# Optimization experiments

Hardware: AMD Instinct MI355X
Metric: run time of the kernel (lower is better)

Reference implementation:

```python
import jax, jax.numpy as jnp
import numpy as np

N_HEAD = 16
D_HEAD = 64
N_GROUPS = 4
D_EMBED = 1024
ROPE_N = 32
B, T = 2, 2048


def apply_rope(x, cos, sin):
    # x: (..., T, ROPE_N); cos/sin: (T, ROPE_N) broadcast over leading dims
    h = x.shape[-1]
    x1, x2 = x[..., : h // 2], x[..., h // 2 :]
    rotated = jnp.concatenate((-x2, x1), axis=-1)
    return (x * cos + rotated * sin).astype(x.dtype)


def setup_inputs() -> dict:
    key = jax.random.key(0)
    k1, k2, k3, k4, k5 = jax.random.split(key, 5)
    return {
        "x": jax.random.normal(k1, (B, T, D_EMBED), dtype=jnp.float32),
        "cos": jax.random.uniform(k2, (T, ROPE_N), dtype=jnp.float32),
        "sin": jax.random.uniform(k3, (T, ROPE_N), dtype=jnp.float32),
        "mask": jnp.ones((B, T), dtype=bool),  # unused by the original forward (passes None to SDPA)
        "Wqkv": jax.random.normal(k4, (D_EMBED, (N_HEAD + 2 * N_GROUPS) * D_HEAD), dtype=jnp.float32) * 0.02,
        "Wout": jax.random.normal(k5, (N_HEAD * D_HEAD, D_EMBED), dtype=jnp.float32) * 0.02,
    }


def reference(x, cos, sin, mask, Wqkv, Wout):
    Bv, Tv, _ = x.shape
    q_per_kv = N_HEAD // N_GROUPS  # 4
    total_qkv = q_per_kv + 2       # 6

    qkv = jnp.einsum("btc,cf->btf", x, Wqkv)  # (B, T, 1536)
    qkv = qkv.reshape(Bv, Tv, N_GROUPS, total_qkv, D_HEAD)
    qkv = jnp.transpose(qkv, (0, 2, 3, 1, 4))  # (B, G, total_qkv, T, d)

    q = qkv[:, :, :q_per_kv]           # (B, G, q_per_kv, T, d)
    k = qkv[:, :, q_per_kv : q_per_kv + 1]  # (B, G, 1, T, d)
    v = qkv[:, :, q_per_kv + 1 :]           # (B, G, 1, T, d)

    # GQA expand (1 < groups < heads)
    k = jnp.broadcast_to(k, (Bv, N_GROUPS, q_per_kv, Tv, D_HEAD))
    v = jnp.broadcast_to(v, (Bv, N_GROUPS, q_per_kv, Tv, D_HEAD))

    q = q.reshape(Bv, N_HEAD, Tv, D_HEAD)
    k = k.reshape(Bv, N_HEAD, Tv, D_HEAD)
    v = v.reshape(Bv, N_HEAD, Tv, D_HEAD)

    # partial RoPE on the first ROPE_N dims of each head
    q = jnp.concatenate((apply_rope(q[..., :ROPE_N], cos, sin), q[..., ROPE_N:]), axis=-1)
    k = jnp.concatenate((apply_rope(k[..., :ROPE_N], cos, sin), k[..., ROPE_N:]), axis=-1)

    scale = 1.0 / np.sqrt(D_HEAD).astype(np.float32)
    scores = jnp.einsum("bhtd,bhsd->bhts", q, k) * scale
    attn = jax.nn.softmax(scores, axis=-1)
    y = jnp.einsum("bhts,bhsd->bhtd", attn, v)   # (B, H, T, d)
    y = jnp.transpose(y, (0, 2, 1, 3)).reshape(Bv, Tv, N_HEAD * D_HEAD)
    return jnp.einsum("btf,fc->btc", y, Wout)
```

## Files before the change

kernel.cpp:

```cpp
#include <hip/hip_runtime.h>
#include <hip/hip_bf16.h>
#include <math.h>

#define BATCH   2
#define TSEQ    2048
#define DEMBED  1024
#define NHEAD   16
#define DHEAD   64
#define NGROUP  4
#define ROPEN   32
#define FQKV    1536
#define MROWS   (BATCH*TSEQ)

typedef __attribute__((ext_vector_type(8))) short short8;
typedef __attribute__((ext_vector_type(4))) float floatx4;

__device__ __forceinline__ void split_pack8(const float* f, uint4& h4, uint4& l4) {
    uint u[8], lu[8];
    #pragma unroll
    for (int j = 0; j < 8; ++j) {
        u[j] = __float_as_uint(f[j]);
        float lf = f[j] - __uint_as_float(u[j] & 0xffff0000u);
        lu[j] = __float_as_uint(lf);
    }
    h4.x = __builtin_amdgcn_perm(u[1], u[0], 0x07060302u);
    h4.y = __builtin_amdgcn_perm(u[3], u[2], 0x07060302u);
    h4.z = __builtin_amdgcn_perm(u[5], u[4], 0x07060302u);
    h4.w = __builtin_amdgcn_perm(u[7], u[6], 0x07060302u);
    l4.x = __builtin_amdgcn_perm(lu[1], lu[0], 0x07060302u);
    l4.y = __builtin_amdgcn_perm(lu[3], lu[2], 0x07060302u);
    l4.z = __builtin_amdgcn_perm(lu[5], lu[4], 0x07060302u);
    l4.w = __builtin_amdgcn_perm(lu[7], lu[6], 0x07060302u);
}

__device__ __forceinline__ void rtn_pack8(const float* f, uint4& h4) {
    uint t[8];
    #pragma unroll
    for (int j = 0; j < 8; ++j)
        t[j] = __float_as_uint(f[j]) + 0x8000u;
    h4.x = __builtin_amdgcn_perm(t[1], t[0], 0x07060302u);
    h4.y = __builtin_amdgcn_perm(t[3], t[2], 0x07060302u);
    h4.z = __builtin_amdgcn_perm(t[5], t[4], 0x07060302u);
    h4.w = __builtin_amdgcn_perm(t[7], t[6], 0x07060302u);
}

__device__ __forceinline__ uint pk_bf16x2(float f0, float f1) {
    uint u0 = __float_as_uint(f0) + 0x8000u;
    uint u1 = __float_as_uint(f1) + 0x8000u;
    return __builtin_amdgcn_perm(u1, u0, 0x07060302u);
}

__device__ __forceinline__ float fast_exp2(float x) {
    float r;
    asm("v_exp_f32 %0, %1" : "=v"(r) : "v"(x));
    return r;
}

__device__ __forceinline__ void lds_async16(void* lds, const void* gp) {
    __builtin_amdgcn_global_load_lds(
        (const __attribute__((address_space(1))) unsigned int*)gp,
        (__attribute__((address_space(3))) unsigned int*)lds,
        16, 0, 0);
}


__global__ __launch_bounds__(256) void conv_xy(const float* __restrict__ in,
                                               char* __restrict__ img) {
    const int tid = threadIdx.x;
    const int c   = blockIdx.x & 15;
    const int mt  = blockIdx.x >> 4;
    const int r    = tid >> 1;
    const int half = tid & 1;

    const float* src = in + (size_t)(mt*128 + r)*1024 + c*64 + half*32;
    float f[32];
    #pragma unroll
    for (int u = 0; u < 8; ++u)
        *(float4*)(f + 4*u) = *(const float4*)(src + 4*u);

    char* tile = img + ((size_t)(mt*16 + c)) * 32768;
    #pragma unroll
    for (int cc = 0; cc < 4; ++cc) {
        uint4 h4, l4;
        split_pack8(f + cc*8, h4, l4);
        int j    = half*4 + cc;
        int phys = j ^ (r & 7);
        *(uint4*)(tile + r*128 + phys*16)         = h4;
        *(uint4*)(tile + 16384 + r*128 + phys*16) = l4;
    }
}

__global__ __launch_bounds__(256) void conv_w(const float* __restrict__ W,
                                              int N,
                                              char* __restrict__ img) {
    __shared__ float Lf[64][132];
    const int tid = threadIdx.x;
    const int c   = blockIdx.x;
    const int nt  = blockIdx.y;

    {
        const int kk = tid >> 2;
        const int nc = (tid & 3) * 32;
        const float* src = W + (size_t)(c*64 + kk)*N + nt*128 + nc;
        #pragma unroll
        for (int u = 0; u < 8; ++u)
            *(float4*)(&Lf[kk][nc + 4*u]) = *(const float4*)(src + 4*u);
    }
    __syncthreads();

    char* tile = img + ((size_t)(nt*16 + c)) * 32768;
    #pragma unroll
    for (int rep = 0; rep < 4; ++rep) {
        int idx = rep*256 + tid;
        int n = idx & 127;
        int j = idx >> 7;
        float v[8];
        #pragma unroll
        for (int i = 0; i < 8; ++i) v[i] = Lf[j*8 + i][n];
        uint4 h4, l4;
        split_pack8(v, h4, l4);
        int phys = j ^ (n & 7);
        *(uint4*)(tile + n*128 + phys*16)         = h4;
        *(uint4*)(tile + 16384 + n*128 + phys*16) = l4;
    }
}

struct GemmAcc { floatx4 a[4][4]; };

__device__ __forceinline__ void gemm_mfma_core(const char* __restrict__ Aimg,
                                               const char* __restrict__ Bimg,
                                               char* smem, int mt, int nt,
                                               int tid, GemmAcc& G) {
    const int wv = tid >> 6;
    const int wm = wv & 1, wn = wv >> 1;
    const int lane = tid & 63;
    const int qd = lane >> 4, cl = lane & 15;
    const int wslot = (tid & 192) * 16;

    #pragma unroll
    for (int tm = 0; tm < 4; ++tm)
        #pragma unroll
        for (int tn = 0; tn < 4; ++tn)
            G.a[tm][tn] = (floatx4){0.f, 0.f, 0.f, 0.f};

    for (int c = 0; c < 16; ++c) {
        __syncthreads();
        {
            const uint4* gA = (const uint4*)(Aimg + ((size_t)(mt*16 + c)) * 32768) + tid;
            const uint4* gB = (const uint4*)(Bimg + ((size_t)(nt*16 + c)) * 32768) + tid;
            #pragma unroll
            for (int j = 0; j < 8; ++j) {
                lds_async16(smem + j*4096 + wslot,         gA + j*256);
                lds_async16(smem + 32768 + j*4096 + wslot, gB + j*256);
            }
        }
        __syncthreads();

        #pragma unroll
        for (int s = 0; s < 2; ++s) {
            const int phys = ((s*4 + qd) ^ (cl & 7)) * 16;
            short8 ah[4], al[4], bh[4], bl[4];
            #pragma unroll
            for (int tt = 0; tt < 4; ++tt) {
                const int rA = wm*64 + 16*tt + cl;
                ah[tt] = *(const short8*)(smem + rA*128 + phys);
                al[tt] = *(const short8*)(smem + 16384 + rA*128 + phys);
                const int rB = wn*64 + 16*tt + cl;
                bh[tt] = *(const short8*)(smem + 32768 + rB*128 + phys);
                bl[tt] = *(const short8*)(smem + 49152 + rB*128 + phys);
            }
            #pragma unroll
            for (int tm = 0; tm < 4; ++tm)
                #pragma unroll
                for (int tn = 0; tn < 4; ++tn) {
                    G.a[tm][tn] = __builtin_amdgcn_mfma_f32_16x16x32_bf16(ah[tm], bh[tn], G.a[tm][tn], 0, 0, 0);
                    G.a[tm][tn] = __builtin_amdgcn_mfma_f32_16x16x32_bf16(al[tm], bh[tn], G.a[tm][tn], 0, 0, 0);
                    G.a[tm][tn] = __builtin_amdgcn_mfma_f32_16x16x32_bf16(ah[tm], bl[tn], G.a[tm][tn], 0, 0, 0);
                }
        }
    }
}

__global__ __launch_bounds__(256, 2) void gemm_qkv_mfma(const char* __restrict__ Aimg,
                                                        const char* __restrict__ Bimg,
                                                        const float* __restrict__ cosp,
                                                        const float* __restrict__ sinp,
                                                        float* __restrict__ Qf,
                                                        ushort* __restrict__ Kimg,
                                                        ushort* __restrict__ Vimg) {
    __shared__ __align__(16) char smem[68608];
    const int tid = threadIdx.x;
    const int nt = blockIdx.x, mt = blockIdx.y;

    GemmAcc G;
    gemm_mfma_core(Aimg, Bimg, smem, mt, nt, tid, G);

    const int wv = tid >> 6;
    const int wm = wv & 1, wn = wv >> 1;
    const int lane = tid & 63;
    const int qd = lane >> 4, cl = lane & 15;

    const int slice = nt*2 + wn;
    const int g  = slice / 6;
    const int jj = slice % 6;
    const int b  = mt >> 4;

    if (jj != 5) {
        #pragma unroll
        for (int tm = 0; tm < 4; ++tm)
            #pragma unroll
            for (int r = 0; r < 4; ++r) {
                int m = mt*128 + wm*64 + 16*tm + 4*qd + r;
                int t = m & 2047;
                float c1 = cosp[t*ROPEN + cl],      s1 = sinp[t*ROPEN + cl];
                float c2 = cosp[t*ROPEN + 16 + cl], s2 = sinp[t*ROPEN + 16 + cl];
                float x1 = G.a[tm][0][r], x2 = G.a[tm][1][r];
                G.a[tm][0][r] = x1*c1 - x2*s1;
                G.a[tm][1][r] = x2*c2 + x1*s2;
            }
    }

    if (jj < 4) {
        #pragma unroll
        for (int tm = 0; tm < 4; ++tm)
            #pragma unroll
            for (int tn = 0; tn < 4; ++tn)
                #pragma unroll
                for (int r = 0; r < 4; ++r) {
                    int m = mt*128 + wm*64 + 16*tm + 4*qd + r;
                    Qf[(size_t)m*1024 + (g*4 + jj)*64 + 16*tn + cl] = G.a[tm][tn][r];
                }
    } else {
        float* Lw = (float*)(smem + wv*17152);
        __syncthreads();
        #pragma unroll
        for (int tm = 0; tm < 4; ++tm)
            #pragma unroll
            for (int tn = 0; tn < 4; ++tn)
                #pragma unroll
                for (int r = 0; r < 4; ++r)
                    Lw[(16*tm + 4*qd + r)*67 + 16*tn + cl] = G.a[tm][tn][r];
        __syncthreads();

        const int cloc = (mt & 15)*2 + wm;
        ushort* img = ((jj == 4) ? Kimg : Vimg)
                      + (size_t)(b*4 + g)*262144 + (size_t)cloc*8192;
        if (jj == 4) {
            const int rr = lane;
            float f[8];
            #pragma unroll
            for (int ch = 0; ch < 8; ++ch) {
                *(float4*)f       = *(const float4*)(&Lw[rr*67 + ch*8]);
                *(float4*)(f + 4) = *(const float4*)(&Lw[rr*67 + ch*8 + 4]);
                uint4 h4, l4;
                split_pack8(f, h4, l4);
                int phys = ch ^ (rr & 7);
                *(uint4*)(img + rr*64 + phys*8)        = h4;
                *(uint4*)(img + 4096 + rr*64 + phys*8) = l4;
            }
        } else {
            const int d = lane;
            float f[8];
            #pragma unroll
            for (int ch = 0; ch < 8; ++ch) {
                const int kb = 32*(ch >> 2) + 4*(ch & 3);
                #pragma unroll
                for (int i = 0; i < 4; ++i) f[i]     = Lw[(kb + i)*67 + d];
                #pragma unroll
                for (int i = 0; i < 4; ++i) f[4 + i] = Lw[(kb + 16 + i)*67 + d];
                uint4 h4;
                rtn_pack8(f, h4);
                int phys = ch ^ (d & 7);
                *(uint4*)(img + d*64 + phys*8) = h4;
            }
        }
    }
}

__global__ __launch_bounds__(256, 2) void gemm_out_mfma(const char* __restrict__ Aimg,
                                                        const char* __restrict__ Bimg,
                                                        float* __restrict__ C) {
    __shared__ __align__(16) char smem[49152];
    const int tid = threadIdx.x;
    const int nt = blockIdx.x, mt = blockIdx.y;

    const int wv = tid >> 6;
    const int wm = wv & 1, wn = wv >> 1;
    const int lane = tid & 63;
    const int qd = lane >> 4, cl = lane & 15;
    const int wslot = (tid & 192) * 16;

    floatx4 acc[2][4];
    #pragma unroll
    for (int tm = 0; tm < 2; ++tm)
        #pragma unroll
        for (int tn = 0; tn < 4; ++tn)
            acc[tm][tn] = (floatx4){0.f, 0.f, 0.f, 0.f};

    for (int c = 0; c < 16; ++c) {
        __syncthreads();
        {
            const char* sA = Aimg + ((size_t)((mt >> 1)*16 + c))*32768
                                  + (mt & 1)*8192 + (size_t)tid*16;
            const char* sB = Bimg + ((size_t)(nt*16 + c))*32768 + (size_t)tid*16;
            lds_async16(smem + wslot,          sA);
            lds_async16(smem + 4096  + wslot,  sA + 4096);
            lds_async16(smem + 8192  + wslot,  sA + 16384);
            lds_async16(smem + 12288 + wslot,  sA + 16384 + 4096);
            #pragma unroll
            for (int j = 0; j < 4; ++j) {
                lds_async16(smem + 16384 + j*4096 + wslot, sB + j*4096);
                lds_async16(smem + 32768 + j*4096 + wslot, sB + 16384 + j*4096);
            }
        }
        __syncthreads();

        #pragma unroll
        for (int s = 0; s < 2; ++s) {
            const int phys = ((s*4 + qd) ^ (cl & 7)) * 16;
            short8 ah[2], al[2], bh[4], bl[4];
            #pragma unroll
            for (int tt = 0; tt < 2; ++tt) {
                const int rA = wm*32 + 16*tt + cl;
                ah[tt] = *(const short8*)(smem + rA*128 + phys);
                al[tt] = *(const short8*)(smem + 8192 + rA*128 + phys);
            }
            #pragma unroll
            for (int tt = 0; tt < 4; ++tt) {
                const int rB = wn*64 + 16*tt + cl;
                bh[tt] = *(const short8*)(smem + 16384 + rB*128 + phys);
                bl[tt] = *(const short8*)(smem + 32768 + rB*128 + phys);
            }
            #pragma unroll
            for (int tm = 0; tm < 2; ++tm)
                #pragma unroll
                for (int tn = 0; tn < 4; ++tn) {
                    acc[tm][tn] = __builtin_amdgcn_mfma_f32_16x16x32_bf16(ah[tm], bh[tn], acc[tm][tn], 0, 0, 0);
                    acc[tm][tn] = __builtin_amdgcn_mfma_f32_16x16x32_bf16(al[tm], bh[tn], acc[tm][tn], 0, 0, 0);
                    acc[tm][tn] = __builtin_amdgcn_mfma_f32_16x16x32_bf16(ah[tm], bl[tn], acc[tm][tn], 0, 0, 0);
                }
        }
    }

    #pragma unroll
    for (int tm = 0; tm < 2; ++tm)
        #pragma unroll
        for (int tn = 0; tn < 4; ++tn)
            #pragma unroll
            for (int r = 0; r < 4; ++r) {
                int m = mt*64 + wm*32 + 16*tm + 4*qd + r;
                int n = nt*128 + wn*64 + 16*tn + cl;
                C[(size_t)m*1024 + n] = acc[tm][tn][r];
            }
}

__global__ __launch_bounds__(256, 4) void attn11(const float* __restrict__ Qf,
                                                 const char* __restrict__ Kimg,
                                                 const char* __restrict__ Vimg,
                                                 char* __restrict__ Yimg) {
    __shared__ __align__(16) char smem[32768];

    const int tid  = threadIdx.x;
    const int wv   = tid >> 6;
    const int lane = tid & 63;
    const int qd   = lane >> 4;
    const int cl   = lane & 15;

    const int bg    = blockIdx.x & 7;
    const int inner = blockIdx.x >> 3;
    const int hj    = inner >> 5;
    const int qt    = inner & 31;
    const int b = bg >> 2, g = bg & 3;
    const int h = g*4 + hj;

    short8 qh[2], ql[2];
    {
        const float* qp = Qf + (size_t)(b*2048 + qt*64 + wv*16 + cl)*1024
                             + h*64 + 8*qd;
        #pragma unroll
        for (int s = 0; s < 2; ++s) {
            float f[8];
            *(float4*)f       = *(const float4*)(qp + 32*s);
            *(float4*)(f + 4) = *(const float4*)(qp + 32*s + 4);
            #pragma unroll
            for (int i = 0; i < 8; ++i) f[i] *= 0.125f * 1.44269504088896f;
            uint4 h4, l4;
            split_pack8(f, h4, l4);
            qh[s] = __builtin_bit_cast(short8, h4);
            ql[s] = __builtin_bit_cast(short8, l4);
        }
    }

    floatx4 accOT[4] = {};
    float lsum = 0.f;

    const char* Kg0 = Kimg + (size_t)bg*524288;
    const char* Vg0 = Vimg + (size_t)bg*524288;
    const int wslot = (tid & 192) * 16;

    int voff[2][4];
    #pragma unroll
    for (int hh = 0; hh < 2; ++hh)
        #pragma unroll
        for (int tt = 0; tt < 4; ++tt)
            voff[hh][tt] = (16*tt + cl)*128 + (((4*hh + qd) ^ (cl & 7))*16);

    {
        const char* src = Kg0 + (size_t)tid*16;
        #pragma unroll
        for (int j = 0; j < 4; ++j)
            lds_async16(smem + j*4096 + wslot, src + j*4096);
    }

    for (int c = 0; c < TSEQ/64; ++c) {
        __syncthreads();
        const int buf = c & 1;
        if (c + 1 < TSEQ/64) {
            const char* src = Kg0 + (size_t)(c+1)*16384 + (size_t)tid*16;
            #pragma unroll
            for (int j = 0; j < 4; ++j)
                lds_async16(smem + (1-buf)*16384 + j*4096 + wslot, src + j*4096);
        }
        const char* Kl = smem + buf*16384;
        const char* Vg = Vg0 + (size_t)c*16384;

        #pragma unroll
        for (int hh = 0; hh < 2; ++hh) {
            short8 vh[4];
            #pragma unroll
            for (int tt = 0; tt < 4; ++tt)
                vh[tt] = *(const short8*)(Vg + voff[hh][tt]);

            floatx4 accST[2] = {};
            __builtin_amdgcn_s_setprio(1);
            #pragma unroll
            for (int s = 0; s < 2; ++s) {
                #pragma unroll
                for (int tt = 0; tt < 2; ++tt) {
                    const int off = (32*hh + 16*tt + cl)*128
                                  + (((4*s + qd) ^ (cl & 7))*16);
                    short8 kh = *(const short8*)(Kl + off);
                    short8 kl = *(const short8*)(Kl + 8192 + off);
                    accST[tt] = __builtin_amdgcn_mfma_f32_16x16x32_bf16(kh, qh[s], accST[tt], 0, 0, 0);
                    accST[tt] = __builtin_amdgcn_mfma_f32_16x16x32_bf16(kh, ql[s], accST[tt], 0, 0, 0);
                    accST[tt] = __builtin_amdgcn_mfma_f32_16x16x32_bf16(kl, qh[s], accST[tt], 0, 0, 0);
                }
            }
            __builtin_amdgcn_s_setprio(0);

            float p[8];
            #pragma unroll
            for (int tt = 0; tt < 2; ++tt)
                #pragma unroll
                for (int r = 0; r < 4; ++r)
                    p[4*tt + r] = fast_exp2(accST[tt][r]);
            lsum += ((p[0] + p[1]) + (p[2] + p[3]))
                  + ((p[4] + p[5]) + (p[6] + p[7]));
            uint4 paw;
            paw.x = pk_bf16x2(p[0], p[1]);
            paw.y = pk_bf16x2(p[2], p[3]);
            paw.z = pk_bf16x2(p[4], p[5]);
            paw.w = pk_bf16x2(p[6], p[7]);
            short8 pa = __builtin_bit_cast(short8, paw);

            __builtin_amdgcn_s_setprio(1);
            #pragma unroll
            for (int tt = 0; tt < 4; ++tt)
                accOT[tt] = __builtin_amdgcn_mfma_f32_16x16x32_bf16(vh[tt], pa, accOT[tt], 0, 0, 0);
            __builtin_amdgcn_s_setprio(0);
        }
    }

    __syncthreads();
    float* Lt = (float*)smem;
    {
        float l = lsum;
        l += __shfl_xor(l, 16);
        l += __shfl_xor(l, 32);
        float inv = 1.0f / l;
        const int row = 16*wv + cl;
        #pragma unroll
        for (int tt = 0; tt < 4; ++tt)
            #pragma unroll
            for (int r = 0; r < 4; ++r)
                Lt[row*66 + 16*tt + 4*qd + r] = accOT[tt][r] * inv;
    }
    __syncthreads();
    {
        const int r0 = tid >> 2;
        const int qq = tid & 3;
        float f[16];
        #pragma unroll
        for (int u = 0; u < 8; ++u)
            *(float2*)(f + 2*u) = *(const float2*)(&Lt[r0*66 + qq*16 + 2*u]);
        const int R = (qt & 1)*64 + r0;
        char* tile = Yimg + (size_t)((b*16 + (qt >> 1))*16 + h) * 32768;
        #pragma unroll
        for (int cc = 0; cc < 2; ++cc) {
            uint4 h4, l4;
            split_pack8(f + 8*cc, h4, l4);
            int j    = qq*2 + cc;
            int phys = j ^ (R & 7);
            *(uint4*)(tile + R*128 + phys*16)         = h4;
            *(uint4*)(tile + 16384 + R*128 + phys*16) = l4;
        }
    }
}

extern "C" void kernel_launch(void* const* d_in, const int* in_sizes, int n_in,
                              void* d_out, int out_size, void* d_ws, size_t ws_size,
                              hipStream_t stream) {
    const float* x    = (const float*)d_in[0];
    const float* cosp = (const float*)d_in[1];
    const float* sinp = (const float*)d_in[2];
    const float* Wqkv = (const float*)d_in[4];
    const float* Wout = (const float*)d_in[5];
    float* out = (float*)d_out;

    char* ws = (char*)d_ws;
    float*  Qf    = (float*)(ws);
    ushort* Kimg  = (ushort*)(ws + ((size_t)16<<20));
    ushort* Vimg  = (ushort*)(ws + ((size_t)20<<20));
    char*   Bo    = ws + ((size_t)24<<20);
    char*   Ximg  = ws + ((size_t)28<<20);
    char*   Bq    = ws + ((size_t)44<<20);
    char*   Yimg  = ws + ((size_t)28<<20);

    conv_xy<<<512, 256, 0, stream>>>(x, Ximg);
    conv_w<<<dim3(16, 12), 256, 0, stream>>>(Wqkv, FQKV, Bq);
    conv_w<<<dim3(16, 8), 256, 0, stream>>>(Wout, DEMBED, Bo);
    gemm_qkv_mfma<<<dim3(12, 32), 256, 0, stream>>>(Ximg, Bq, cosp, sinp,
                                                    Qf, Kimg, Vimg);
    attn11<<<1024, 256, 0, stream>>>(Qf, (const char*)Kimg, (const char*)Vimg,
                                     Yimg);
    gemm_out_mfma<<<dim3(8, 64), 256, 0, stream>>>(Yimg, Bo, out);
}
```

Before: 243.4 us.

## Split attention key chunks across two wave groups with LDS reduction

The attention kernel now runs 512 threads per block. Two groups of four waves each process one half of every 64-key chunk, where before one wave handled both halves in sequence. Partial output accumulators and row sums from the second group are reduced through shared memory before normalisation and the final bf16 hi/lo store. This doubles the waves available to hide MFMA and memory latency. In exchange it adds an extra LDS reduction pass, more shared memory and a larger block that may limit occupancy.

```diff
diff --git a/kernel.cpp b/kernel.cpp
--- a/kernel.cpp
+++ b/kernel.cpp
@@ -354,14 +354,16 @@
             }
 }
 
-__global__ __launch_bounds__(256, 4) void attn11(const float* __restrict__ Qf,
+__global__ __launch_bounds__(512, 8) void attn12(const float* __restrict__ Qf,
                                                  const char* __restrict__ Kimg,
                                                  const char* __restrict__ Vimg,
                                                  char* __restrict__ Yimg) {
-    __shared__ __align__(16) char smem[32768];
+    __shared__ __align__(16) char smem[34816];
 
     const int tid  = threadIdx.x;
-    const int wv   = tid >> 6;
+    const int wv8  = tid >> 6;
+    const int grp  = wv8 >> 2;
+    const int wq   = wv8 & 3;
     const int lane = tid & 63;
     const int qd   = lane >> 4;
     const int cl   = lane & 15;
@@ -375,7 +377,7 @@
 
     short8 qh[2], ql[2];
     {
-        const float* qp = Qf + (size_t)(b*2048 + qt*64 + wv*16 + cl)*1024
+        const float* qp = Qf + (size_t)(b*2048 + qt*64 + wq*16 + cl)*1024
                              + h*64 + 8*qd;
         #pragma unroll
         for (int s = 0; s < 2; ++s) {
@@ -396,89 +398,100 @@
 
     const char* Kg0 = Kimg + (size_t)bg*524288;
     const char* Vg0 = Vimg + (size_t)bg*524288;
-    const int wslot = (tid & 192) * 16;
-
-    int voff[2][4];
-    #pragma unroll
-    for (int hh = 0; hh < 2; ++hh)
-        #pragma unroll
-        for (int tt = 0; tt < 4; ++tt)
-            voff[hh][tt] = (16*tt + cl)*128 + (((4*hh + qd) ^ (cl & 7))*16);
+    const int wslot = wv8 << 10;
+
+    int voff[4];
+    #pragma unroll
+    for (int tt = 0; tt < 4; ++tt)
+        voff[tt] = (16*tt + cl)*128 + (((4*grp + qd) ^ (cl & 7))*16);
 
     {
         const char* src = Kg0 + (size_t)tid*16;
-        #pragma unroll
-        for (int j = 0; j < 4; ++j)
-            lds_async16(smem + j*4096 + wslot, src + j*4096);
+        lds_async16(smem + wslot,        src);
+        lds_async16(smem + 8192 + wslot, src + 8192);
     }
 
     for (int c = 0; c < TSEQ/64; ++c) {
         __syncthreads();
         const int buf = c & 1;
+        const char* Vg = Vg0 + (size_t)c*16384;
+
+        short8 vh[4];
+        #pragma unroll
+        for (int tt = 0; tt < 4; ++tt)
+            vh[tt] = *(const short8*)(Vg + voff[tt]);
+
         if (c + 1 < TSEQ/64) {
             const char* src = Kg0 + (size_t)(c+1)*16384 + (size_t)tid*16;
-            #pragma unroll
-            for (int j = 0; j < 4; ++j)
-                lds_async16(smem + (1-buf)*16384 + j*4096 + wslot, src + j*4096);
+            lds_async16(smem + (1-buf)*16384 + wslot,        src);
+            lds_async16(smem + (1-buf)*16384 + 8192 + wslot, src + 8192);
         }
         const char* Kl = smem + buf*16384;
-        const char* Vg = Vg0 + (size_t)c*16384;
-
-        #pragma unroll
-        for (int hh = 0; hh < 2; ++hh) {
-            short8 vh[4];
-            #pragma unroll
-            for (int tt = 0; tt < 4; ++tt)
-                vh[tt] = *(const short8*)(Vg + voff[hh][tt]);
-
-            floatx4 accST[2] = {};
-            __builtin_amdgcn_s_setprio(1);
-            #pragma unroll
-            for (int s = 0; s < 2; ++s) {
-                #pragma unroll
-                for (int tt = 0; tt < 2; ++tt) {
-                    const int off = (32*hh + 16*tt + cl)*128
-                                  + (((4*s + qd) ^ (cl & 7))*16);
-                    short8 kh = *(const short8*)(Kl + off);
-                    short8 kl = *(const short8*)(Kl + 8192 + off);
-                    accST[tt] = __builtin_amdgcn_mfma_f32_16x16x32_bf16(kh, qh[s], accST[tt], 0, 0, 0);
-                    accST[tt] = __builtin_amdgcn_mfma_f32_16x16x32_bf16(kh, ql[s], accST[tt], 0, 0, 0);
-                    accST[tt] = __builtin_amdgcn_mfma_f32_16x16x32_bf16(kl, qh[s], accST[tt], 0, 0, 0);
-                }
-            }
-            __builtin_amdgcn_s_setprio(0);
-
-            float p[8];
-            #pragma unroll
-            for (int tt = 0; tt < 2; ++tt)
-                #pragma unroll
-                for (int r = 0; r < 4; ++r)
-                    p[4*tt + r] = fast_exp2(accST[tt][r]);
-            lsum += ((p[0] + p[1]) + (p[2] + p[3]))
-                  + ((p[4] + p[5]) + (p[6] + p[7]));
-            uint4 paw;
-            paw.x = pk_bf16x2(p[0], p[1]);
-            paw.y = pk_bf16x2(p[2], p[3]);
-            paw.z = pk_bf16x2(p[4], p[5]);
-            paw.w = pk_bf16x2(p[6], p[7]);
-            short8 pa = __builtin_bit_cast(short8, paw);
-
-            __builtin_amdgcn_s_setprio(1);
-            #pragma unroll
-            for (int tt = 0; tt < 4; ++tt)
-                accOT[tt] = __builtin_amdgcn_mfma_f32_16x16x32_bf16(vh[tt], pa, accOT[tt], 0, 0, 0);
-            __builtin_amdgcn_s_setprio(0);
-        }
+
+        floatx4 accST[2] = {};
+        __builtin_amdgcn_s_setprio(1);
+        #pragma unroll
+        for (int s = 0; s < 2; ++s) {
+            #pragma unroll
+            for (int tt = 0; tt < 2; ++tt) {
+                const int off = (32*grp + 16*tt + cl)*128
+                              + (((4*s + qd) ^ (cl & 7))*16);
+                short8 kh = *(const short8*)(Kl + off);
+                short8 kl = *(const short8*)(Kl + 8192 + off);
+                accST[tt] = __builtin_amdgcn_mfma_f32_16x16x32_bf16(kh, qh[s], accST[tt], 0, 0, 0);
+                accST[tt] = __builtin_amdgcn_mfma_f32_16x16x32_bf16(kh, ql[s], accST[tt], 0, 0, 0);
+                accST[tt] = __builtin_amdgcn_mfma_f32_16x16x32_bf16(kl, qh[s], accST[tt], 0, 0, 0);
+            }
+        }
+        __builtin_amdgcn_s_setprio(0);
+
+        float p[8];
+        #pragma unroll
+        for (int tt = 0; tt < 2; ++tt)
+            #pragma unroll
+            for (int r = 0; r < 4; ++r)
+                p[4*tt + r] = fast_exp2(accST[tt][r]);
+        lsum += ((p[0] + p[1]) + (p[2] + p[3]))
+              + ((p[4] + p[5]) + (p[6] + p[7]));
+        uint4 paw;
+        paw.x = pk_bf16x2(p[0], p[1]);
+        paw.y = pk_bf16x2(p[2], p[3]);
+        paw.z = pk_bf16x2(p[4], p[5]);
+        paw.w = pk_bf16x2(p[6], p[7]);
+        short8 pa = __builtin_bit_cast(short8, paw);
+
+        __builtin_amdgcn_s_setprio(1);
+        #pragma unroll
+        for (int tt = 0; tt < 4; ++tt)
+            accOT[tt] = __builtin_amdgcn_mfma_f32_16x16x32_bf16(vh[tt], pa, accOT[tt], 0, 0, 0);
+        __builtin_amdgcn_s_setprio(0);
     }
 
     __syncthreads();
-    float* Lt = (float*)smem;
-    {
-        float l = lsum;
+    float* Pb = (float*)smem;
+    if (grp == 1) {
+        float* dst = Pb + (size_t)(wq*64 + lane)*17;
+        #pragma unroll
+        for (int tt = 0; tt < 4; ++tt)
+            #pragma unroll
+            for (int r = 0; r < 4; ++r)
+                dst[4*tt + r] = accOT[tt][r];
+        dst[16] = lsum;
+    }
+    __syncthreads();
+    float* Lt = (float*)(smem + 17920);
+    if (grp == 0) {
+        const float* sp = Pb + (size_t)(wq*64 + lane)*17;
+        #pragma unroll
+        for (int tt = 0; tt < 4; ++tt)
+            #pragma unroll
+            for (int r = 0; r < 4; ++r)
+                accOT[tt][r] += sp[4*tt + r];
+        float l = lsum + sp[16];
         l += __shfl_xor(l, 16);
         l += __shfl_xor(l, 32);
         float inv = 1.0f / l;
-        const int row = 16*wv + cl;
+        const int row = 16*wq + cl;
         #pragma unroll
         for (int tt = 0; tt < 4; ++tt)
             #pragma unroll
@@ -487,23 +500,19 @@
     }
     __syncthreads();
     {
-        const int r0 = tid >> 2;
-        const int qq = tid & 3;
-        float f[16];
-        #pragma unroll
-        for (int u = 0; u < 8; ++u)
-            *(float2*)(f + 2*u) = *(const float2*)(&Lt[r0*66 + qq*16 + 2*u]);
+        const int r0 = tid >> 3;
+        const int qq = tid & 7;
+        float f[8];
+        #pragma unroll
+        for (int u = 0; u < 4; ++u)
+            *(float2*)(f + 2*u) = *(const float2*)(&Lt[r0*66 + qq*8 + 2*u]);
         const int R = (qt & 1)*64 + r0;
         char* tile = Yimg + (size_t)((b*16 + (qt >> 1))*16 + h) * 32768;
-        #pragma unroll
-        for (int cc = 0; cc < 2; ++cc) {
-            uint4 h4, l4;
-            split_pack8(f + 8*cc, h4, l4);
-            int j    = qq*2 + cc;
-            int phys = j ^ (R & 7);
-            *(uint4*)(tile + R*128 + phys*16)         = h4;
-            *(uint4*)(tile + 16384 + R*128 + phys*16) = l4;
-        }
+        uint4 h4, l4;
+        split_pack8(f, h4, l4);
+        int phys = qq ^ (R & 7);
+        *(uint4*)(tile + R*128 + phys*16)         = h4;
+        *(uint4*)(tile + 16384 + R*128 + phys*16) = l4;
     }
 }
 
@@ -531,7 +540,7 @@
     conv_w<<<dim3(16, 8), 256, 0, stream>>>(Wout, DEMBED, Bo);
     gemm_qkv_mfma<<<dim3(12, 32), 256, 0, stream>>>(Ximg, Bq, cosp, sinp,
                                                     Qf, Kimg, Vimg);
-    attn11<<<1024, 256, 0, stream>>>(Qf, (const char*)Kimg, (const char*)Vimg,
+    attn12<<<1024, 512, 0, stream>>>(Qf, (const char*)Kimg, (const char*)Vimg,
                                      Yimg);
     gemm_out_mfma<<<dim3(8, 64), 256, 0, stream>>>(Yimg, Bo, out);
 }
```

Result: slower. 377.0 us (+54.9%).
